# Performance work log

Measured on AMD Instinct MI355X. Metric: run time of the kernel, lower is better.

## Reference

```python
import jax, jax.numpy as jnp
import numpy as np

EMBED = 2048
NUM_HEADS = 32
HEAD_DIM = EMBED // NUM_HEADS  # 64 (original head dim; sets the scaling)
RANK_KQ = 1024
RANK_V = 1024
DK = RANK_KQ // NUM_HEADS  # 32 low-rank kq head dim
DV = RANK_V // NUM_HEADS   # 32 low-rank v head dim
B, S = 2, 2048


def setup_inputs() -> dict:
    key = jax.random.key(0)
    ks = jax.random.split(key, 10)
    std = 0.02
    hidden_states = jax.random.normal(ks[0], (B, S, EMBED), dtype=jnp.float32)
    # causal additive mask, shape (B, 1, S, S) as asserted in forward
    neg = jnp.finfo(jnp.float32).min
    causal = jnp.where(jnp.tril(jnp.ones((S, S), dtype=bool)), 0.0, neg)
    attention_mask = jnp.broadcast_to(causal[None, None], (B, 1, S, S)).astype(jnp.float32)
    Wq = jax.random.normal(ks[1], (RANK_KQ, EMBED), dtype=jnp.float32) * std
    bq = jax.random.normal(ks[2], (RANK_KQ,), dtype=jnp.float32) * std
    Wk = jax.random.normal(ks[3], (RANK_KQ, EMBED), dtype=jnp.float32) * std
    bk = jax.random.normal(ks[4], (RANK_KQ,), dtype=jnp.float32) * std
    Wv = jax.random.normal(ks[5], (RANK_V, EMBED), dtype=jnp.float32) * std
    bv = jax.random.normal(ks[6], (RANK_V,), dtype=jnp.float32) * std
    Wo = jax.random.normal(ks[7], (EMBED, RANK_V), dtype=jnp.float32) * std
    bo = jax.random.normal(ks[8], (EMBED,), dtype=jnp.float32) * std
    return {"hidden_states": hidden_states, "attention_mask": attention_mask,
            "Wq": Wq, "bq": bq, "Wk": Wk, "bk": bk, "Wv": Wv, "bv": bv,
            "Wo": Wo, "bo": bo}


def reference(hidden_states, attention_mask, Wq, bq, Wk, bk, Wv, bv, Wo, bo):
    bsz, tgt_len, _ = hidden_states.shape
    scaling = HEAD_DIM ** (-0.5)  # uses ORIGINAL head_dim, not low-rank dim

    def split_heads(x, d):  # (b, s, H*d) -> (b, H, s, d)
        return x.reshape(bsz, -1, NUM_HEADS, d).transpose(0, 2, 1, 3)

    q = split_heads((hidden_states @ Wq.T + bq) * scaling, DK)
    k = split_heads(hidden_states @ Wk.T + bk, DK)
    v = split_heads(hidden_states @ Wv.T + bv, DV)

    # scores: (b, H, tgt, src)
    attn = jnp.einsum('bhqd,bhkd->bhqk', q, k)
    attn = attn + attention_mask  # broadcast over heads
    attn = jnp.maximum(attn, jnp.finfo(attn.dtype).min)
    attn = jax.nn.softmax(attn, axis=-1)

    out = jnp.einsum('bhqk,bhkd->bhqd', attn, v)  # (b, H, tgt, DV)
    out = out.transpose(0, 2, 1, 3).reshape(bsz, tgt_len, RANK_V)
    return out @ Wo.T + bo
```

## Files before the change

kernel.cpp:

```cpp
#include <hip/hip_runtime.h>
#include <stdint.h>

typedef __attribute__((ext_vector_type(8))) short bf16x8;
typedef __attribute__((ext_vector_type(4))) float f32x4;
typedef unsigned short ushort_t;

#define AS1 __attribute__((address_space(1)))
#define AS3 __attribute__((address_space(3)))

static __device__ __forceinline__ ushort_t f2b(float f) {
    union { float f; unsigned u; } x; x.f = f;
    unsigned r = x.u + 0x7fffu + ((x.u >> 16) & 1u);
    return (ushort_t)(r >> 16);
}
static __device__ __forceinline__ f32x4 mfma16(bf16x8 a, bf16x8 b, f32x4 c) {
    return __builtin_amdgcn_mfma_f32_16x16x32_bf16(a, b, c, 0, 0, 0);
}
static __device__ __forceinline__ void gl_lds16(const ushort_t* g, ushort_t* l) {
    __builtin_amdgcn_global_load_lds((const AS1 void*)g, (AS3 void*)l, 16, 0, 0);
}
static __device__ __forceinline__ unsigned pk2(float a, float b) {
    unsigned r;
    asm("v_cvt_pk_bf16_f32 %0, %1, %2" : "=v"(r) : "v"(a), "v"(b));
    return r;
}

__global__ __launch_bounds__(256)
void cvt_bf16(const float* __restrict__ s, ushort_t* __restrict__ d, int n8)
{
    int i = blockIdx.x * 256 + threadIdx.x;
    if (i >= n8) return;
    const float* p = s + (size_t)i * 8;
    f32x4 a = *(const f32x4*)p;
    f32x4 b = *(const f32x4*)(p + 4);
    bf16x8 r;
#pragma unroll
    for (int j = 0; j < 4; ++j) { r[j] = (short)f2b(a[j]); r[j+4] = (short)f2b(b[j]); }
    *(bf16x8*)(d + (size_t)i * 8) = r;
}

__global__ __launch_bounds__(256)
void cvt_w3(const float* __restrict__ wq, const float* __restrict__ wk,
            const float* __restrict__ wv, ushort_t* __restrict__ d)
{
    const float* s = (blockIdx.y == 0) ? wq : (blockIdx.y == 1) ? wk : wv;
    ushort_t* dst = d + (size_t)blockIdx.y * 2097152;
    int i = blockIdx.x * 256 + threadIdx.x;
    const float* p = s + (size_t)i * 8;
    f32x4 a = *(const f32x4*)p;
    f32x4 b = *(const f32x4*)(p + 4);
    bf16x8 r;
#pragma unroll
    for (int j = 0; j < 4; ++j) { r[j] = (short)f2b(a[j]); r[j+4] = (short)f2b(b[j]); }
    *(bf16x8*)(dst + (size_t)i * 8) = r;
}

__global__ __launch_bounds__(512, 1)
void gemm8c(const ushort_t* __restrict__ A, const ushort_t* __restrict__ B,
            const float* __restrict__ b0, const float* __restrict__ b1,
            const float* __restrict__ b2, void* __restrict__ Cv,
            int M, int N, int K)
{
    __shared__ __align__(16) ushort_t lds[65536];
    const int tid = threadIdx.x;
    const int wave = tid >> 6, lane = tid & 63;
    const int l16 = lane & 15, quad = lane >> 4;
    const int wr = wave >> 2, wc = wave & 3;
    const int bm = blockIdx.x * 128, bn = blockIdx.y * 384;
    const int xo = (l16 & 8) << 1;
    const int S = K >> 4;
    const int NT = K >> 7;

    f32x4 acc[4][6];
#pragma unroll
    for (int i = 0; i < 4; ++i)
#pragma unroll
        for (int j = 0; j < 6; ++j) acc[i][j] = (f32x4){0.f,0.f,0.f,0.f};

    auto stg = [&](int s_) {
        int slot = s_ & 7;
        ushort_t* base = lds + (slot >> 1) * 16384;
        int ko = (s_ >> 1) << 5;
        if (s_ & 1) {
            int c = tid;
            int cl = c ^ (((c >> 5) & 1) << 1);
            gl_lds16(A + (size_t)(bm + (cl >> 2)) * K + ko + (cl & 3) * 8,
                     base + 12288 + c * 8);
        } else {
#pragma unroll
            for (int call = 0; call < 3; ++call) {
                int c = call * 512 + tid;
                int cl = c ^ (((c >> 5) & 1) << 1);
                gl_lds16(B + (size_t)(bn + (cl >> 2)) * K + ko + (cl & 3) * 8,
                         base + c * 8);
            }
        }
    };

#pragma unroll
    for (int s0 = 0; s0 < 6; ++s0) stg(s0);
    asm volatile("s_waitcnt vmcnt(8)" ::: "memory");
    __builtin_amdgcn_s_barrier();

    for (int t = 0; t < NT; ++t) {
        const bool lastit = (t == NT - 1);
        bf16x8 bfr[6], af[4];
#pragma unroll
        for (int P = 0; P < 4; ++P) {
            asm volatile("" ::: "memory");
            const int offB = P * 16384;
            const int offA = offB + 12288;
#pragma unroll
            for (int j = 0; j < 6; ++j)
                bfr[j] = *(const bf16x8*)(lds + offB
                          + (wc * 96 + j * 16 + l16) * 32 + ((quad * 8) ^ xo));
#pragma unroll
            for (int m = 0; m < 4; ++m)
                af[m] = *(const bf16x8*)(lds + offA
                          + (wr * 64 + m * 16 + l16) * 32 + ((quad * 8) ^ xo));
            {
                int s1 = 8 * t + 6 + 2 * P;
                if (s1 < S) stg(s1);
                int s2 = s1 + 1;
                if (s2 < S) stg(s2);
            }
            __builtin_amdgcn_s_barrier();
            asm volatile("s_waitcnt lgkmcnt(0)" ::: "memory");
            __builtin_amdgcn_sched_barrier(0);
            __builtin_amdgcn_s_setprio(1);
#pragma unroll
            for (int m = 0; m < 4; ++m)
#pragma unroll
                for (int j = 0; j < 6; ++j)
                    acc[m][j] = mfma16(af[m], bfr[j], acc[m][j]);
            __builtin_amdgcn_s_setprio(0);
            if (!lastit)      asm volatile("s_waitcnt vmcnt(8)" ::: "memory");
            else if (P == 0)  asm volatile("s_waitcnt vmcnt(0)" ::: "memory");
            __builtin_amdgcn_s_barrier();
        }
    }

#pragma unroll
    for (int i = 0; i < 4; ++i) {
#pragma unroll
        for (int j = 0; j < 6; ++j) {
            int col = bn + wc * 96 + j * 16 + l16;
            int mat = col >> 10, nc = col & 1023;
            const float* bp = (mat == 0) ? b0 : (mat == 1) ? b1 : b2;
            float bvs = bp[nc];
            int h = nc >> 5, d = nc & 31;
            if (mat == 2) {
                int row0 = bm + wr * 64 + i * 16 + quad * 4;
                int b = row0 >> 11, s2 = row0 & 2047;
                ushort_t* dst = (ushort_t*)Cv + (size_t)2 * 4194304
                              + ((size_t)(b * 32 + h) * 32 + d) * 2048 + s2;
                uint2 w;
                w.x = ((unsigned)f2b(acc[i][j][1] + bvs) << 16) | f2b(acc[i][j][0] + bvs);
                w.y = ((unsigned)f2b(acc[i][j][3] + bvs) << 16) | f2b(acc[i][j][2] + bvs);
                *(uint2*)dst = w;
            } else {
                float sc = (mat == 0) ? 0.125f : 1.0f;
                ushort_t* dst = (ushort_t*)Cv + (size_t)mat * 4194304;
#pragma unroll
                for (int r = 0; r < 4; ++r) {
                    int row = bm + wr * 64 + i * 16 + quad * 4 + r;
                    int b = row >> 11, s2 = row & 2047;
                    float v = (acc[i][j][r] + bvs) * sc;
                    dst[(((size_t)(b * 32 + h) * 2048 + s2) << 5) + d] = f2b(v);
                }
            }
        }
    }
}

__global__ __launch_bounds__(512, 1)
void gemm8b(const ushort_t* __restrict__ A, const ushort_t* __restrict__ B,
            const float* __restrict__ bias, float* __restrict__ C,
            int M, int N, int K, float scale)
{
    __shared__ __align__(16) ushort_t lds[49152];
    const int tid = threadIdx.x;
    const int wave = tid >> 6, lane = tid & 63;
    const int l16 = lane & 15, quad = lane >> 4;
    const int wr = wave >> 2, wc = wave & 3;
    const int bm = blockIdx.x * 128, bn = blockIdx.y * 256;
    const int xo = (l16 & 8) << 1;
    const int S = K >> 4;
    const int NT = K >> 7;

    f32x4 acc[4][4];
#pragma unroll
    for (int i = 0; i < 4; ++i)
#pragma unroll
        for (int j = 0; j < 4; ++j) acc[i][j] = (f32x4){0.f,0.f,0.f,0.f};

    auto stg = [&](int s_) {
        int r = s_ & 7;
        ushort_t* ldst = lds + (r >> 1) * 12288 + (r & 1) * 8192;
        int ko = (s_ >> 1) << 5;
        if (s_ & 1) {
            int c = tid;
            int cl = c ^ (((c >> 5) & 1) << 1);
            gl_lds16(A + (size_t)(bm + (cl >> 2)) * K + ko + (cl & 3) * 8,
                     ldst + c * 8);
        } else {
#pragma unroll
            for (int call = 0; call < 2; ++call) {
                int c = call * 512 + tid;
                int cl = c ^ (((c >> 5) & 1) << 1);
                gl_lds16(B + (size_t)(bn + (cl >> 2)) * K + ko + (cl & 3) * 8,
                         ldst + c * 8);
            }
        }
    };

#pragma unroll
    for (int s0 = 0; s0 < 7; ++s0) stg(s0);
    asm volatile("s_waitcnt vmcnt(5)" ::: "memory");
    __builtin_amdgcn_s_barrier();

    for (int t = 0; t < NT; ++t) {
        const bool lastit = (t == NT - 1);
        bf16x8 bfr[4], af[2];
#pragma unroll
        for (int p = 0; p < 8; ++p) {
            asm volatile("" ::: "memory");
            const int offB = (p >> 1) * 12288;
            const int offA = offB + 8192;
            if ((p & 1) == 0) {
#pragma unroll
                for (int j = 0; j < 4; ++j)
                    bfr[j] = *(const bf16x8*)(lds + offB
                              + (wc * 64 + j * 16 + l16) * 32 + ((quad * 8) ^ xo));
            }
#pragma unroll
            for (int m = 0; m < 2; ++m)
                af[m] = *(const bf16x8*)(lds + offA
                          + (wr * 64 + (p & 1) * 32 + m * 16 + l16) * 32
                          + ((quad * 8) ^ xo));
            { int s_ = 8 * t + 7 + p; if (s_ < S) stg(s_); }
            __builtin_amdgcn_s_barrier();
            asm volatile("s_waitcnt lgkmcnt(0)" ::: "memory");
            __builtin_amdgcn_sched_barrier(0);
            __builtin_amdgcn_s_setprio(1);
#pragma unroll
            for (int m = 0; m < 2; ++m)
#pragma unroll
                for (int j = 0; j < 4; ++j)
                    acc[(p & 1) * 2 + m][j] =
                        mfma16(af[m], bfr[j], acc[(p & 1) * 2 + m][j]);
            __builtin_amdgcn_s_setprio(0);
            if (p == 3) {
                if (lastit) asm volatile("s_waitcnt vmcnt(0)" ::: "memory");
                else        asm volatile("s_waitcnt vmcnt(5)" ::: "memory");
            } else if (p == 7) {
                if (!lastit) asm volatile("s_waitcnt vmcnt(5)" ::: "memory");
            }
            __builtin_amdgcn_s_barrier();
        }
    }

#pragma unroll
    for (int i = 0; i < 4; ++i) {
#pragma unroll
        for (int j = 0; j < 4; ++j) {
            int col = bn + wc * 64 + j * 16 + l16;
            float bvs = bias[col];
#pragma unroll
            for (int r = 0; r < 4; ++r) {
                int row = bm + wr * 64 + i * 16 + quad * 4 + r;
                C[(size_t)row * N + col] = (acc[i][j][r] + bvs) * scale;
            }
        }
    }
}

__global__ __launch_bounds__(256, 4)
void attn(const ushort_t* __restrict__ Q, const ushort_t* __restrict__ Kg,
          const ushort_t* __restrict__ VT, ushort_t* __restrict__ Ctx)
{
    __shared__ __align__(16) ushort_t Ps[4][32 * 72];
    const int tid = threadIdx.x, wave = tid >> 6, lane = tid & 63;
    const int l16 = lane & 15, quad = lane >> 4, quad4 = quad * 4;
    const int bh = blockIdx.x;
    const int pr = blockIdx.y;
    const ushort_t* Qh = Q  + (size_t)bh * 2048 * 32;
    const ushort_t* Kh = Kg + (size_t)bh * 2048 * 32;
    const ushort_t* Vh = VT + (size_t)bh * 32 * 2048;
    const int b = bh >> 5, h = bh & 31;
    ushort_t* P0 = &Ps[wave][0];

    for (int half = 0; half < 2; ++half) {
        const int qt = half ? (15 - pr) : pr;
        const int q0 = qt * 128 + wave * 32;

        bf16x8 qf0 = *(const bf16x8*)(Qh + (size_t)(q0 + l16) * 32 + quad * 8);
        bf16x8 qf1 = *(const bf16x8*)(Qh + (size_t)(q0 + 16 + l16) * 32 + quad * 8);

        f32x4 o00 = (f32x4){0.f,0.f,0.f,0.f}, o01 = o00, o10 = o00, o11 = o00;
        float rs0 = 0.f, rs1 = 0.f;

        const int nchw = ((q0 + 31) >> 6) + 1;
        for (int c = 0; c < nchw; ++c) {
            const int kv0 = c * 64;
            bf16x8 kf[4];
#pragma unroll
            for (int t = 0; t < 4; ++t)
                kf[t] = *(const bf16x8*)(Kh + (size_t)(kv0 + t * 16 + l16) * 32 + quad * 8);
            f32x4 st0[4], st1[4];
#pragma unroll
            for (int t = 0; t < 4; ++t) {
                st0[t] = mfma16(kf[t], qf0, (f32x4){0.f,0.f,0.f,0.f});
                st1[t] = mfma16(kf[t], qf1, (f32x4){0.f,0.f,0.f,0.f});
            }
            bf16x8 vA0 = *(const bf16x8*)(Vh + (size_t)l16 * 2048 + kv0 + quad * 8);
            bf16x8 vA1 = *(const bf16x8*)(Vh + (size_t)l16 * 2048 + kv0 + 32 + quad * 8);
            bf16x8 vB0 = *(const bf16x8*)(Vh + (size_t)(16 + l16) * 2048 + kv0 + quad * 8);
            bf16x8 vB1 = *(const bf16x8*)(Vh + (size_t)(16 + l16) * 2048 + kv0 + 32 + quad * 8);

            const int qk0 = q0 + l16 - kv0;
            auto softmax_pack = [&](bool masked) {
#pragma unroll
                for (int t = 0; t < 4; ++t) {
                    float p0[4], p1[4];
#pragma unroll
                    for (int r = 0; r < 4; ++r) {
                        const int kk = t * 16 + quad4 + r;
                        float e0 = __expf(st0[t][r]);
                        float e1 = __expf(st1[t][r]);
                        p0[r] = (!masked || kk <= qk0)      ? e0 : 0.f;
                        p1[r] = (!masked || kk <= qk0 + 16) ? e1 : 0.f;
                        rs0 += p0[r]; rs1 += p1[r];
                    }
                    uint2 w0, w1;
                    w0.x = pk2(p0[0], p0[1]); w0.y = pk2(p0[2], p0[3]);
                    w1.x = pk2(p1[0], p1[1]); w1.y = pk2(p1[2], p1[3]);
                    *(uint2*)(P0 + (size_t)l16 * 72 + t * 16 + quad4) = w0;
                    *(uint2*)(P0 + (size_t)(16 + l16) * 72 + t * 16 + quad4) = w1;
                }
            };
            if (kv0 + 63 <= q0) softmax_pack(false); else softmax_pack(true);

            asm volatile("s_waitcnt lgkmcnt(0)" ::: "memory");
#pragma unroll
            for (int ks = 0; ks < 2; ++ks) {
                bf16x8 pa0 = *(const bf16x8*)(P0 + (size_t)l16 * 72 + ks * 32 + quad * 8);
                bf16x8 pa1 = *(const bf16x8*)(P0 + (size_t)(16 + l16) * 72 + ks * 32 + quad * 8);
                bf16x8 va = ks ? vA1 : vA0;
                bf16x8 vb = ks ? vB1 : vB0;
                o00 = mfma16(pa0, va, o00);
                o01 = mfma16(pa0, vb, o01);
                o10 = mfma16(pa1, va, o10);
                o11 = mfma16(pa1, vb, o11);
            }
        }

        rs0 += __shfl_xor(rs0, 16); rs0 += __shfl_xor(rs0, 32);
        rs1 += __shfl_xor(rs1, 16); rs1 += __shfl_xor(rs1, 32);

#pragma unroll
        for (int r = 0; r < 4; ++r) {
            const int qr = q0 + quad4 + r;
            float inv0 = 1.0f / __shfl(rs0, quad4 + r);
            float inv1 = 1.0f / __shfl(rs1, quad4 + r);
            size_t base0 = ((size_t)b * 2048 + qr) * 1024 + h * 32;
            size_t base1 = ((size_t)b * 2048 + qr + 16) * 1024 + h * 32;
            Ctx[base0 + l16]      = f2b(o00[r] * inv0);
            Ctx[base0 + 16 + l16] = f2b(o01[r] * inv0);
            Ctx[base1 + l16]      = f2b(o10[r] * inv1);
            Ctx[base1 + 16 + l16] = f2b(o11[r] * inv1);
        }
    }
}

extern "C" void kernel_launch(void* const* d_in, const int* in_sizes, int n_in,
                              void* d_out, int out_size, void* d_ws, size_t ws_size,
                              hipStream_t stream)
{
    const float* H  = (const float*)d_in[0];
    const float* Wq = (const float*)d_in[2];
    const float* bq = (const float*)d_in[3];
    const float* Wk = (const float*)d_in[4];
    const float* bk = (const float*)d_in[5];
    const float* Wv = (const float*)d_in[6];
    const float* bv = (const float*)d_in[7];
    const float* Wo = (const float*)d_in[8];
    const float* bo = (const float*)d_in[9];

    ushort_t* Hb   = (ushort_t*)d_ws;
    ushort_t* Wcat = Hb   + (size_t)8388608;
    ushort_t* Qb   = Wcat + (size_t)6291456;
    ushort_t* Kb   = Qb   + (size_t)4194304;
    ushort_t* Vtb  = Kb   + (size_t)4194304;
    ushort_t* Ctx  = Vtb  + (size_t)4194304;
    ushort_t* Wob  = Hb;

    dim3 blk(256, 1, 1);
    hipLaunchKernelGGL(cvt_bf16, dim3(4096, 1, 1), blk, 0, stream, H, Hb, 1048576);
    hipLaunchKernelGGL(cvt_w3, dim3(1024, 3, 1), blk, 0, stream, Wq, Wk, Wv, Wcat);

    hipLaunchKernelGGL(gemm8c, dim3(32, 8, 1), dim3(512, 1, 1), 0, stream,
                       Hb, Wcat, bq, bk, bv, (void*)Qb, 4096, 3072, 2048);

    hipLaunchKernelGGL(cvt_bf16, dim3(1024, 1, 1), blk, 0, stream, Wo, Wob, 262144);

    hipLaunchKernelGGL(attn, dim3(64, 8, 1), blk, 0, stream, Qb, Kb, Vtb, Ctx);

    hipLaunchKernelGGL(gemm8b, dim3(32, 8, 1), dim3(512, 1, 1), 0, stream,
                       Ctx, Wob, bo, (float*)d_out, 4096, 2048, 1024, 1.0f);
}
```

Measured before the change: 274.6 us.

## Double-buffer LDS fragment reads in registers to overlap with MFMA

The projection GEMM main loop now keeps two register sets of A/B fragments. It loads the next phase's fragments from LDS while the MFMAs run on the current phase, instead of reading and then waiting before each compute block. The barrier between the fragment reads and the global-to-LDS staging is dropped, and the vmcnt waits are tightened from 8 to 4 to match the new ordering. This aims to hide LDS latency behind matrix math, at the cost of more VGPRs and tighter reasoning about buffer hazards.

```diff
diff --git a/kernel.cpp b/kernel.cpp
--- a/kernel.cpp
+++ b/kernel.cpp
@@ -96,46 +96,54 @@
             }
         }
     };
+    auto rdB = [&](int pp, int j) {
+        return *(const bf16x8*)(lds + pp * 16384
+                 + (wc * 96 + j * 16 + l16) * 32 + ((quad * 8) ^ xo));
+    };
+    auto rdA = [&](int pp, int m) {
+        return *(const bf16x8*)(lds + pp * 16384 + 12288
+                 + (wr * 64 + m * 16 + l16) * 32 + ((quad * 8) ^ xo));
+    };
 
 #pragma unroll
     for (int s0 = 0; s0 < 6; ++s0) stg(s0);
-    asm volatile("s_waitcnt vmcnt(8)" ::: "memory");
+    asm volatile("s_waitcnt vmcnt(4)" ::: "memory");
     __builtin_amdgcn_s_barrier();
+
+    bf16x8 bfr[2][6], af[2][4];
+#pragma unroll
+    for (int j = 0; j < 6; ++j) bfr[0][j] = rdB(0, j);
+#pragma unroll
+    for (int m = 0; m < 4; ++m) af[0][m] = rdA(0, m);
+    asm volatile("s_waitcnt lgkmcnt(0)" ::: "memory");
 
     for (int t = 0; t < NT; ++t) {
         const bool lastit = (t == NT - 1);
-        bf16x8 bfr[6], af[4];
 #pragma unroll
         for (int P = 0; P < 4; ++P) {
             asm volatile("" ::: "memory");
-            const int offB = P * 16384;
-            const int offA = offB + 12288;
-#pragma unroll
-            for (int j = 0; j < 6; ++j)
-                bfr[j] = *(const bf16x8*)(lds + offB
-                          + (wc * 96 + j * 16 + l16) * 32 + ((quad * 8) ^ xo));
-#pragma unroll
-            for (int m = 0; m < 4; ++m)
-                af[m] = *(const bf16x8*)(lds + offA
-                          + (wr * 64 + m * 16 + l16) * 32 + ((quad * 8) ^ xo));
+            const int cur = P & 1, nxt = cur ^ 1;
+            const int np = (P + 1) & 3;
+#pragma unroll
+            for (int j = 0; j < 6; ++j) bfr[nxt][j] = rdB(np, j);
+#pragma unroll
+            for (int m = 0; m < 4; ++m) af[nxt][m] = rdA(np, m);
             {
                 int s1 = 8 * t + 6 + 2 * P;
                 if (s1 < S) stg(s1);
                 int s2 = s1 + 1;
                 if (s2 < S) stg(s2);
             }
-            __builtin_amdgcn_s_barrier();
+            __builtin_amdgcn_s_setprio(1);
+#pragma unroll
+            for (int m = 0; m < 4; ++m)
+#pragma unroll
+                for (int j = 0; j < 6; ++j)
+                    acc[m][j] = mfma16(af[cur][m], bfr[cur][j], acc[m][j]);
+            __builtin_amdgcn_s_setprio(0);
             asm volatile("s_waitcnt lgkmcnt(0)" ::: "memory");
-            __builtin_amdgcn_sched_barrier(0);
-            __builtin_amdgcn_s_setprio(1);
-#pragma unroll
-            for (int m = 0; m < 4; ++m)
-#pragma unroll
-                for (int j = 0; j < 6; ++j)
-                    acc[m][j] = mfma16(af[m], bfr[j], acc[m][j]);
-            __builtin_amdgcn_s_setprio(0);
-            if (!lastit)      asm volatile("s_waitcnt vmcnt(8)" ::: "memory");
-            else if (P == 0)  asm volatile("s_waitcnt vmcnt(0)" ::: "memory");
+            if (lastit) asm volatile("s_waitcnt vmcnt(0)" ::: "memory");
+            else        asm volatile("s_waitcnt vmcnt(4)" ::: "memory");
             __builtin_amdgcn_s_barrier();
         }
     }
```

Result: no change. 271.8 us (-1.0%).
